# Performance work log

Measured on AMD Instinct MI355X. Metric: run time of the kernel, lower is better.

The kernel has to match this reference:

```python
import jax, jax.numpy as jnp
import numpy as np

B, N_CLASS, N_CENTER, HIDDEN = 1024, 50, 8, 512
INIT_MU, BETA, EPS = 0.1, 0.5, 1e-8


def setup_inputs() -> dict:
    key = jax.random.key(0)
    k1, k2, k3, k4 = jax.random.split(key, 4)
    x = jax.random.normal(k1, (B, HIDDEN), dtype=jnp.float32)
    # class_mu ~ U(-init_mu, init_mu), matching torch.rand(...) * 2*init_mu - init_mu
    class_mu = jax.random.uniform(k2, (N_CLASS, N_CENTER, HIDDEN),
                                  minval=-INIT_MU, maxval=INIT_MU, dtype=jnp.float32)
    # binary dropout-style mask: (rand > beta).float()
    mask = (jax.random.uniform(k3, (N_CENTER, HIDDEN)) > BETA).astype(jnp.float32)
    # fixed random projection W ~ 0.1 * N(0,1)
    W = jax.random.normal(k4, (HIDDEN, HIDDEN), dtype=jnp.float32) * 0.1
    return {"x": x, "class_mu": class_mu, "mask": mask, "W": W}


def reference(x, class_mu, mask, W):
    # [B, n_center, hidden]: per-center masked copy of x, then shared projection W
    masked = x[:, None, :] * mask[None, :, :]
    mul = jnp.einsum('bch,hd->bcd', masked, W)
    # broadcast squared-distance against cluster centers: [B, n_class, n_center]
    diff = mul[:, None, :, :] - class_mu[None, :, :, :]  # [B, K, C, H]
    score = 1.0 / (1.0 + jnp.sum(diff * diff, axis=-1))  # Student-t style kernel
    # normalize over n_center (dim 2)
    distances = score / (jnp.sum(score, axis=2, keepdims=True) + EPS)
    # k_assign: second normalization over last dim (n_center)
    k_assign = distances / jnp.sum(distances, axis=-1, keepdims=True)
    return (mul, k_assign, distances)
```

## Files before the change

### kernel.cpp

```cpp
#include <hip/hip_runtime.h>

typedef short s16x8 __attribute__((ext_vector_type(8)));
typedef float f32x4 __attribute__((ext_vector_type(4)));

#define NB      1024
#define NCLASS  50
#define NCENTER 8
#define HID     512
#define KPAD    64

#define OFF_WT     0u
#define OFF_MUBF   524288u
#define OFF_MUNORM 1048576u

#define OUT_KA 4194304
#define OUT_D  4603904

__device__ __forceinline__ short f2bf(float f) {
    unsigned int u = __float_as_uint(f);
    unsigned int r = (u + 0x7FFFu + ((u >> 16) & 1u)) >> 16;
    return (short)(unsigned short)r;
}

__global__ __launch_bounds__(256) void prep_kernel(
    const float* __restrict__ class_mu, const float* __restrict__ W,
    short* __restrict__ WT, short* __restrict__ Mubf, float* __restrict__ Munorm)
{
    __shared__ float lds[64][65];
    const int blk = blockIdx.x, tid = threadIdx.x;

    if (blk < 64) {
        int th = blk & 7, td = blk >> 3;
        int col = tid & 63, rb = tid >> 6;
        #pragma unroll
        for (int it = 0; it < 16; ++it) {
            int row = it * 4 + rb;
            lds[row][col] = W[(th * 64 + row) * HID + td * 64 + col];
        }
        __syncthreads();
        #pragma unroll
        for (int it = 0; it < 16; ++it) {
            int row = it * 4 + rb;
            WT[(td * 64 + row) * HID + th * 64 + col] = f2bf(lds[col][row]);
        }
    } else {
        int w = (blk - 64) * 4 + (tid >> 6);
        int lane = tid & 63;
        int c = w >> 6, kk = w & 63;
        int h = lane * 8;
        float v[8];
        if (kk < NCLASS) {
            const float4* p = (const float4*)(class_mu + (kk * NCENTER + c) * HID + h);
            float4 a = p[0], bq = p[1];
            v[0] = a.x;  v[1] = a.y;  v[2] = a.z;  v[3] = a.w;
            v[4] = bq.x; v[5] = bq.y; v[6] = bq.z; v[7] = bq.w;
        } else {
            #pragma unroll
            for (int j = 0; j < 8; ++j) v[j] = 0.f;
        }
        s16x8 o; float sq = 0.f;
        #pragma unroll
        for (int j = 0; j < 8; ++j) { o[j] = f2bf(v[j]); sq += v[j] * v[j]; }
        *(s16x8*)(Mubf + (c * KPAD + kk) * HID + h) = o;
        sq += __shfl_xor(sq, 1);  sq += __shfl_xor(sq, 2);  sq += __shfl_xor(sq, 4);
        sq += __shfl_xor(sq, 8);  sq += __shfl_xor(sq, 16); sq += __shfl_xor(sq, 32);
        if (lane == 0) Munorm[c * KPAD + kk] = sq;
    }
}

__global__ __launch_bounds__(256) void gemm_mul(
    const float* __restrict__ x, const float* __restrict__ mask,
    const short* __restrict__ WT, float* __restrict__ mul_out)
{
    __shared__ short As[64 * 32];
    __shared__ short Bs[128 * 32];
    const int tid = threadIdx.x;
    const int bm = blockIdx.x * 64;
    const int bn = blockIdx.y * 128;
    const int wave = tid >> 6, lane = tid & 63;
    const int wm = (wave & 1) * 32, wn = (wave >> 1) * 64;
    const int q = lane >> 4, l16 = lane & 15;

    f32x4 acc[2][4] = {};

    const int r0 = tid >> 2, c0 = (tid & 3) * 8;
    const int xr = (bm >> 3) + (r0 >> 3);
    const float* xp = x + xr * HID + c0;
    const float* mp = mask + (r0 & 7) * HID + c0;
    const short* wp = WT + (bn + r0) * HID + c0;

    float4 xa, xb, ma, mb; s16x8 w0, w1;
#define GLOAD(IT) do { const int kq = (IT) * 32; \
        xa = *(const float4*)(xp + kq); xb = *(const float4*)(xp + kq + 4); \
        ma = *(const float4*)(mp + kq); mb = *(const float4*)(mp + kq + 4); \
        w0 = *(const s16x8*)(wp + kq);  w1 = *(const s16x8*)(wp + 64 * HID + kq); } while (0)

    GLOAD(0);
    #pragma unroll
    for (int it = 0; it < 16; ++it) {
        s16x8 oa;
        oa[0] = f2bf(xa.x * ma.x); oa[1] = f2bf(xa.y * ma.y);
        oa[2] = f2bf(xa.z * ma.z); oa[3] = f2bf(xa.w * ma.w);
        oa[4] = f2bf(xb.x * mb.x); oa[5] = f2bf(xb.y * mb.y);
        oa[6] = f2bf(xb.z * mb.z); oa[7] = f2bf(xb.w * mb.w);
        s16x8 cw0 = w0, cw1 = w1;
        if (it < 15) GLOAD(it + 1);

        __syncthreads();
        *(s16x8*)(As + r0 * 32 + c0)        = oa;
        *(s16x8*)(Bs + r0 * 32 + c0)        = cw0;
        *(s16x8*)(Bs + (r0 + 64) * 32 + c0) = cw1;
        __syncthreads();

        s16x8 af[2], bfr[4];
        #pragma unroll
        for (int mt = 0; mt < 2; ++mt)
            af[mt] = *(const s16x8*)(As + (wm + mt * 16 + l16) * 32 + q * 8);
        #pragma unroll
        for (int nt = 0; nt < 4; ++nt)
            bfr[nt] = *(const s16x8*)(Bs + (wn + nt * 16 + l16) * 32 + q * 8);
        #pragma unroll
        for (int mt = 0; mt < 2; ++mt)
            #pragma unroll
            for (int nt = 0; nt < 4; ++nt)
                acc[mt][nt] = __builtin_amdgcn_mfma_f32_16x16x32_bf16(af[mt], bfr[nt], acc[mt][nt], 0, 0, 0);
    }
#undef GLOAD

    #pragma unroll
    for (int mt = 0; mt < 2; ++mt)
        #pragma unroll
        for (int nt = 0; nt < 4; ++nt)
            #pragma unroll
            for (int reg = 0; reg < 4; ++reg) {
                int gr = bm + wm + mt * 16 + q * 4 + reg;
                int gc = bn + wn + nt * 16 + l16;
                mul_out[gr * HID + gc] = acc[mt][nt][reg];
            }
}

__global__ __launch_bounds__(512) void score_norm_kernel(
    const float* __restrict__ mul, const short* __restrict__ Mubf,
    const float* __restrict__ Munorm, float* __restrict__ out)
{
    __shared__ float sc[16][16][9];
    const int tid = threadIdx.x;
    const int bt = blockIdx.x >> 2, kt = blockIdx.x & 3;
    const int b0 = bt * 16, kbase = kt * 16;
    const int c = tid >> 6;
    const int lane = tid & 63;
    const int q = lane >> 4, l16 = lane & 15;

    f32x4 acc = {};
    float nrm = 0.f;

    const float* arow = mul + ((b0 + l16) * NCENTER + c) * HID + q * 8;
    const short* brow = Mubf + (c * KPAD + kbase + l16) * HID + q * 8;

    #pragma unroll 4
    for (int it = 0; it < 16; ++it) {
        const int k0 = it * 32;
        float4 a0 = *(const float4*)(arow + k0);
        float4 a1 = *(const float4*)(arow + k0 + 4);
        s16x8 bv = *(const s16x8*)(brow + k0);
        s16x8 av;
        av[0] = f2bf(a0.x); av[1] = f2bf(a0.y); av[2] = f2bf(a0.z); av[3] = f2bf(a0.w);
        av[4] = f2bf(a1.x); av[5] = f2bf(a1.y); av[6] = f2bf(a1.z); av[7] = f2bf(a1.w);
        nrm += a0.x * a0.x + a0.y * a0.y + a0.z * a0.z + a0.w * a0.w
             + a1.x * a1.x + a1.y * a1.y + a1.z * a1.z + a1.w * a1.w;
        acc = __builtin_amdgcn_mfma_f32_16x16x32_bf16(av, bv, acc, 0, 0, 0);
    }

    nrm += __shfl_xor(nrm, 16);
    nrm += __shfl_xor(nrm, 32);

    float mn = Munorm[c * KPAD + kbase + l16];
    #pragma unroll
    for (int reg = 0; reg < 4; ++reg) {
        float rn = __shfl(nrm, q * 4 + reg);
        float sq = rn + mn - 2.f * acc[reg];
        sc[q * 4 + reg][l16][c] = 1.f / (1.f + sq);
    }
    __syncthreads();

    if (tid < 256) {
        int b = tid >> 4, k = tid & 15;
        int kcls = kbase + k;
        if (kcls < NCLASS) {
            float s0 = sc[b][k][0], s1 = sc[b][k][1], s2 = sc[b][k][2], s3 = sc[b][k][3];
            float s4 = sc[b][k][4], s5 = sc[b][k][5], s6 = sc[b][k][6], s7 = sc[b][k][7];
            float S = ((s0 + s1) + (s2 + s3)) + ((s4 + s5) + (s6 + s7));
            float invd = 1.f / (S + 1e-8f);
            float invk = 1.f / S;
            float* kap = out + OUT_KA + ((b0 + b) * NCLASS + kcls) * NCENTER;
            float* dp  = out + OUT_D  + ((b0 + b) * NCLASS + kcls) * NCENTER;
            float4 ka0 = {s0 * invk, s1 * invk, s2 * invk, s3 * invk};
            float4 ka1 = {s4 * invk, s5 * invk, s6 * invk, s7 * invk};
            float4 dd0 = {s0 * invd, s1 * invd, s2 * invd, s3 * invd};
            float4 dd1 = {s4 * invd, s5 * invd, s6 * invd, s7 * invd};
            ((float4*)kap)[0] = ka0; ((float4*)kap)[1] = ka1;
            ((float4*)dp)[0]  = dd0; ((float4*)dp)[1]  = dd1;
        }
    }
}

extern "C" void kernel_launch(void* const* d_in, const int* in_sizes, int n_in,
                              void* d_out, int out_size, void* d_ws, size_t ws_size,
                              hipStream_t stream) {
    const float* x        = (const float*)d_in[0];
    const float* class_mu = (const float*)d_in[1];
    const float* mask     = (const float*)d_in[2];
    const float* W        = (const float*)d_in[3];
    float* out = (float*)d_out;
    char* ws = (char*)d_ws;

    short* WT     = (short*)(ws + OFF_WT);
    short* Mubf   = (short*)(ws + OFF_MUBF);
    float* Munorm = (float*)(ws + OFF_MUNORM);

    prep_kernel<<<192, 256, 0, stream>>>(class_mu, W, WT, Mubf, Munorm);
    gemm_mul<<<dim3(128, 4), 256, 0, stream>>>(x, mask, WT, out);
    score_norm_kernel<<<256, 512, 0, stream>>>(out, Mubf, Munorm, out);
}
```

Before: 93.68 us.

## Fuse prep, GEMM and score into one cooperative kernel with grid syncs

Merges the three launches into a single cooperative kernel of 512 blocks that uses grid-wide syncs between the prep, GEMM and score phases, with a fallback to separate launches if the cooperative launch fails. The GEMM now also writes a bf16 copy of mul, which the score phase reads instead of converting fp32 itself. Each score wave handles two centers. The GEMM LDS rows are padded to a stride of 40 to cut bank conflicts, and block indices are swizzled. This removes launch gaps and halves the score-phase read traffic, but adds grid-barrier cost and an extra bf16 store.

```diff
diff --git a/kernel.cpp b/kernel.cpp
--- a/kernel.cpp
+++ b/kernel.cpp
@@ -1,4 +1,7 @@
 #include <hip/hip_runtime.h>
+#include <hip/hip_cooperative_groups.h>
+
+namespace cg = cooperative_groups;
 
 typedef short s16x8 __attribute__((ext_vector_type(8)));
 typedef float f32x4 __attribute__((ext_vector_type(4)));
@@ -12,24 +15,29 @@
 #define OFF_WT     0u
 #define OFF_MUBF   524288u
 #define OFF_MUNORM 1048576u
+#define OFF_MULBF  1050624u
 
 #define OUT_KA 4194304
 #define OUT_D  4603904
+
+#define ASTR 40
+#define SMEM_BYTES 16640
 
 __device__ __forceinline__ short f2bf(float f) {
     unsigned int u = __float_as_uint(f);
     unsigned int r = (u + 0x7FFFu + ((u >> 16) & 1u)) >> 16;
     return (short)(unsigned short)r;
 }
-
-__global__ __launch_bounds__(256) void prep_kernel(
+__device__ __forceinline__ float bf2f(short h) {
+    return __uint_as_float(((unsigned int)(unsigned short)h) << 16);
+}
+
+__device__ __forceinline__ void prep_body(int blk, int tid, char* smem,
     const float* __restrict__ class_mu, const float* __restrict__ W,
     short* __restrict__ WT, short* __restrict__ Mubf, float* __restrict__ Munorm)
 {
-    __shared__ float lds[64][65];
-    const int blk = blockIdx.x, tid = threadIdx.x;
-
     if (blk < 64) {
+        float (*lds)[65] = (float (*)[65])smem;
         int th = blk & 7, td = blk >> 3;
         int col = tid & 63, rb = tid >> 6;
         #pragma unroll
@@ -43,7 +51,7 @@
             int row = it * 4 + rb;
             WT[(td * 64 + row) * HID + th * 64 + col] = f2bf(lds[col][row]);
         }
-    } else {
+    } else if (blk < 192) {
         int w = (blk - 64) * 4 + (tid >> 6);
         int lane = tid & 63;
         int c = w >> 6, kk = w & 63;
@@ -68,15 +76,16 @@
     }
 }
 
-__global__ __launch_bounds__(256) void gemm_mul(
+__device__ __forceinline__ void gemm_body(int blk, int tid, char* smem,
     const float* __restrict__ x, const float* __restrict__ mask,
-    const short* __restrict__ WT, float* __restrict__ mul_out)
-{
-    __shared__ short As[64 * 32];
-    __shared__ short Bs[128 * 32];
-    const int tid = threadIdx.x;
-    const int bm = blockIdx.x * 64;
-    const int bn = blockIdx.y * 128;
+    const short* __restrict__ WT, float* __restrict__ mul_out,
+    short* __restrict__ mulbf)
+{
+    short* As = (short*)smem;
+    short* Bs = (short*)smem + 64 * ASTR;
+    const int swz = (blk & 7) * 64 + (blk >> 3);
+    const int bm = (swz >> 2) * 64;
+    const int bn = (swz & 3) * 128;
     const int wave = tid >> 6, lane = tid & 63;
     const int wm = (wave & 1) * 32, wn = (wave >> 1) * 64;
     const int q = lane >> 4, l16 = lane & 15;
@@ -107,18 +116,18 @@
         if (it < 15) GLOAD(it + 1);
 
         __syncthreads();
-        *(s16x8*)(As + r0 * 32 + c0)        = oa;
-        *(s16x8*)(Bs + r0 * 32 + c0)        = cw0;
-        *(s16x8*)(Bs + (r0 + 64) * 32 + c0) = cw1;
+        *(s16x8*)(As + r0 * ASTR + c0)        = oa;
+        *(s16x8*)(Bs + r0 * ASTR + c0)        = cw0;
+        *(s16x8*)(Bs + (r0 + 64) * ASTR + c0) = cw1;
         __syncthreads();
 
         s16x8 af[2], bfr[4];
         #pragma unroll
         for (int mt = 0; mt < 2; ++mt)
-            af[mt] = *(const s16x8*)(As + (wm + mt * 16 + l16) * 32 + q * 8);
+            af[mt] = *(const s16x8*)(As + (wm + mt * 16 + l16) * ASTR + q * 8);
         #pragma unroll
         for (int nt = 0; nt < 4; ++nt)
-            bfr[nt] = *(const s16x8*)(Bs + (wn + nt * 16 + l16) * 32 + q * 8);
+            bfr[nt] = *(const s16x8*)(Bs + (wn + nt * 16 + l16) * ASTR + q * 8);
         #pragma unroll
         for (int mt = 0; mt < 2; ++mt)
             #pragma unroll
@@ -135,55 +144,61 @@
             for (int reg = 0; reg < 4; ++reg) {
                 int gr = bm + wm + mt * 16 + q * 4 + reg;
                 int gc = bn + wn + nt * 16 + l16;
-                mul_out[gr * HID + gc] = acc[mt][nt][reg];
+                float v = acc[mt][nt][reg];
+                mul_out[gr * HID + gc] = v;
+                mulbf[gr * HID + gc] = f2bf(v);
             }
 }
 
-__global__ __launch_bounds__(512) void score_norm_kernel(
-    const float* __restrict__ mul, const short* __restrict__ Mubf,
+__device__ __forceinline__ void score_body(int blk, int tid, char* smem,
+    const short* __restrict__ mulbf, const short* __restrict__ Mubf,
     const float* __restrict__ Munorm, float* __restrict__ out)
 {
-    __shared__ float sc[16][16][9];
-    const int tid = threadIdx.x;
-    const int bt = blockIdx.x >> 2, kt = blockIdx.x & 3;
+    if (blk >= 256) return;
+    float (*sc)[16][9] = (float (*)[16][9])smem;
+    const int bt = blk >> 2, kt = blk & 3;
     const int b0 = bt * 16, kbase = kt * 16;
-    const int c = tid >> 6;
-    const int lane = tid & 63;
+    const int wave = tid >> 6, lane = tid & 63;
     const int q = lane >> 4, l16 = lane & 15;
-
-    f32x4 acc = {};
-    float nrm = 0.f;
-
-    const float* arow = mul + ((b0 + l16) * NCENTER + c) * HID + q * 8;
-    const short* brow = Mubf + (c * KPAD + kbase + l16) * HID + q * 8;
+    const int ca = wave * 2, cb = ca + 1;
+
+    f32x4 acc0 = {}, acc1 = {};
+    float nrm0 = 0.f, nrm1 = 0.f;
+
+    const short* arow = mulbf + ((b0 + l16) * NCENTER + ca) * HID + q * 8;
+    const short* brow = Mubf + (ca * KPAD + kbase + l16) * HID + q * 8;
 
     #pragma unroll 4
     for (int it = 0; it < 16; ++it) {
         const int k0 = it * 32;
-        float4 a0 = *(const float4*)(arow + k0);
-        float4 a1 = *(const float4*)(arow + k0 + 4);
-        s16x8 bv = *(const s16x8*)(brow + k0);
-        s16x8 av;
-        av[0] = f2bf(a0.x); av[1] = f2bf(a0.y); av[2] = f2bf(a0.z); av[3] = f2bf(a0.w);
-        av[4] = f2bf(a1.x); av[5] = f2bf(a1.y); av[6] = f2bf(a1.z); av[7] = f2bf(a1.w);
-        nrm += a0.x * a0.x + a0.y * a0.y + a0.z * a0.z + a0.w * a0.w
-             + a1.x * a1.x + a1.y * a1.y + a1.z * a1.z + a1.w * a1.w;
-        acc = __builtin_amdgcn_mfma_f32_16x16x32_bf16(av, bv, acc, 0, 0, 0);
-    }
-
-    nrm += __shfl_xor(nrm, 16);
-    nrm += __shfl_xor(nrm, 32);
-
-    float mn = Munorm[c * KPAD + kbase + l16];
+        s16x8 a0 = *(const s16x8*)(arow + k0);
+        s16x8 a1 = *(const s16x8*)(arow + HID + k0);
+        s16x8 bv0 = *(const s16x8*)(brow + k0);
+        s16x8 bv1 = *(const s16x8*)(brow + KPAD * HID + k0);
+        #pragma unroll
+        for (int j = 0; j < 8; ++j) {
+            float f0 = bf2f(a0[j]); nrm0 += f0 * f0;
+            float f1 = bf2f(a1[j]); nrm1 += f1 * f1;
+        }
+        acc0 = __builtin_amdgcn_mfma_f32_16x16x32_bf16(a0, bv0, acc0, 0, 0, 0);
+        acc1 = __builtin_amdgcn_mfma_f32_16x16x32_bf16(a1, bv1, acc1, 0, 0, 0);
+    }
+
+    nrm0 += __shfl_xor(nrm0, 16); nrm0 += __shfl_xor(nrm0, 32);
+    nrm1 += __shfl_xor(nrm1, 16); nrm1 += __shfl_xor(nrm1, 32);
+
+    float mn0 = Munorm[ca * KPAD + kbase + l16];
+    float mn1 = Munorm[cb * KPAD + kbase + l16];
     #pragma unroll
     for (int reg = 0; reg < 4; ++reg) {
-        float rn = __shfl(nrm, q * 4 + reg);
-        float sq = rn + mn - 2.f * acc[reg];
-        sc[q * 4 + reg][l16][c] = 1.f / (1.f + sq);
+        float rn0 = __shfl(nrm0, q * 4 + reg);
+        float rn1 = __shfl(nrm1, q * 4 + reg);
+        sc[q * 4 + reg][l16][ca] = 1.f / (1.f + rn0 + mn0 - 2.f * acc0[reg]);
+        sc[q * 4 + reg][l16][cb] = 1.f / (1.f + rn1 + mn1 - 2.f * acc1[reg]);
     }
     __syncthreads();
 
-    if (tid < 256) {
+    {
         int b = tid >> 4, k = tid & 15;
         int kcls = kbase + k;
         if (kcls < NCLASS) {
@@ -204,6 +219,43 @@
     }
 }
 
+__global__ void __launch_bounds__(256, 2) fused_kernel(
+    const float* __restrict__ x, const float* __restrict__ class_mu,
+    const float* __restrict__ mask, const float* __restrict__ W,
+    short* __restrict__ WT, short* __restrict__ Mubf, float* __restrict__ Munorm,
+    short* __restrict__ mulbf, float* __restrict__ out)
+{
+    __shared__ __align__(16) char smem[SMEM_BYTES];
+    cg::grid_group grid = cg::this_grid();
+    prep_body(blockIdx.x, threadIdx.x, smem, class_mu, W, WT, Mubf, Munorm);
+    grid.sync();
+    gemm_body(blockIdx.x, threadIdx.x, smem, x, mask, WT, out, mulbf);
+    grid.sync();
+    score_body(blockIdx.x, threadIdx.x, smem, mulbf, Mubf, Munorm, out);
+}
+
+__global__ void __launch_bounds__(256) prep_sep(
+    const float* __restrict__ class_mu, const float* __restrict__ W,
+    short* __restrict__ WT, short* __restrict__ Mubf, float* __restrict__ Munorm)
+{
+    __shared__ __align__(16) char smem[SMEM_BYTES];
+    prep_body(blockIdx.x, threadIdx.x, smem, class_mu, W, WT, Mubf, Munorm);
+}
+__global__ void __launch_bounds__(256) gemm_sep(
+    const float* __restrict__ x, const float* __restrict__ mask,
+    const short* __restrict__ WT, float* __restrict__ mul_out, short* __restrict__ mulbf)
+{
+    __shared__ __align__(16) char smem[SMEM_BYTES];
+    gemm_body(blockIdx.x, threadIdx.x, smem, x, mask, WT, mul_out, mulbf);
+}
+__global__ void __launch_bounds__(256) score_sep(
+    const short* __restrict__ mulbf, const short* __restrict__ Mubf,
+    const float* __restrict__ Munorm, float* __restrict__ out)
+{
+    __shared__ __align__(16) char smem[SMEM_BYTES];
+    score_body(blockIdx.x, threadIdx.x, smem, mulbf, Mubf, Munorm, out);
+}
+
 extern "C" void kernel_launch(void* const* d_in, const int* in_sizes, int n_in,
                               void* d_out, int out_size, void* d_ws, size_t ws_size,
                               hipStream_t stream) {
@@ -217,8 +269,17 @@
     short* WT     = (short*)(ws + OFF_WT);
     short* Mubf   = (short*)(ws + OFF_MUBF);
     float* Munorm = (float*)(ws + OFF_MUNORM);
-
-    prep_kernel<<<192, 256, 0, stream>>>(class_mu, W, WT, Mubf, Munorm);
-    gemm_mul<<<dim3(128, 4), 256, 0, stream>>>(x, mask, WT, out);
-    score_norm_kernel<<<256, 512, 0, stream>>>(out, Mubf, Munorm, out);
-}
+    short* mulbf  = (short*)(ws + OFF_MULBF);
+
+    void* args[] = { (void*)&x, (void*)&class_mu, (void*)&mask, (void*)&W,
+                     (void*)&WT, (void*)&Mubf, (void*)&Munorm, (void*)&mulbf,
+                     (void*)&out };
+    hipError_t err = hipLaunchCooperativeKernel((const void*)fused_kernel,
+                                                dim3(512), dim3(256), args, 0, stream);
+    if (err != hipSuccess) {
+        (void)hipGetLastError();
+        prep_sep<<<192, 256, 0, stream>>>(class_mu, W, WT, Mubf, Munorm);
+        gemm_sep<<<512, 256, 0, stream>>>(x, mask, WT, out, mulbf);
+        score_sep<<<256, 256, 0, stream>>>(mulbf, Mubf, Munorm, out);
+    }
+}
```

New measurement: 230.8 us. +146.4%, slower.
